# Kernel tuning notes

Hardware: AMD Instinct MI355X
Metric: run time of the kernel (lower is better)

The kernel has to match this reference:

```python
import jax, jax.numpy as jnp
import numpy as np

B, ENC, DEC, H, W = 8, 64, 128, 128, 128
NEG = -1e30  # masked-softmax fill


def _neighbors(x):
    """x: [B,H,W,C] -> [B,H,W,9,C] 3x3 neighborhood gather (zeros at borders)."""
    b, h, w, c = x.shape
    p = jnp.pad(x, ((0, 0), (1, 1), (1, 1), (0, 0)))
    return jnp.stack([p[:, r:r + h, c_:c_ + w, :] for r in range(3) for c_ in range(3)], axis=3)


def _neighbor_mask(h, w):
    """[H,W,9] bool: which of the 9 neighbors are in-bounds per pixel."""
    m = jnp.pad(jnp.ones((h, w), dtype=bool), ((1, 1), (1, 1)))
    return jnp.stack([m[r:r + h, c_:c_ + w] for r in range(3) for c_ in range(3)], axis=2)


def setup_inputs() -> dict:
    key = jax.random.key(0)
    ks = jax.random.split(key, 12)
    s = 0.05
    return {
        "encoder_features": jax.random.normal(ks[0], (B, ENC, H, W), jnp.float32),
        "decoder_features": jax.random.normal(ks[1], (B, DEC, H, W), jnp.float32),
        "W_enc": jax.random.normal(ks[2], (ENC, ENC), jnp.float32) * s,
        "b_enc": jax.random.normal(ks[3], (ENC,), jnp.float32) * s,
        "W_dec": jax.random.normal(ks[4], (DEC, ENC), jnp.float32) * s,
        "b_dec": jax.random.normal(ks[5], (ENC,), jnp.float32) * s,
        "W_agg": jax.random.normal(ks[6], (ENC, 1), jnp.float32) * s,
        "b_agg": jax.random.normal(ks[7], (1,), jnp.float32) * s,
        "W_attn": jax.random.normal(ks[8], (2 * ENC, ENC), jnp.float32) * s,
        "b_attn": jax.random.normal(ks[9], (ENC,), jnp.float32) * s,
        "conv_w": jax.random.normal(ks[10], (3, 3, DEC, ENC), jnp.float32) * s,  # HWIO
        "conv_b": jax.random.normal(ks[11], (ENC,), jnp.float32) * s,
    }


def reference(encoder_features, decoder_features, W_enc, b_enc, W_dec, b_dec,
              W_agg, b_agg, W_attn, b_attn, conv_w, conv_b):
    # NCHW -> NHWC (format_linear)
    enc = jnp.transpose(encoder_features, (0, 2, 3, 1))  # [B,H,W,ENC]
    dec = jnp.transpose(decoder_features, (0, 2, 3, 1))  # [B,H,W,DEC]

    q = dec @ W_dec + b_dec  # [B,H,W,ENC]
    k = enc @ W_enc + b_enc  # [B,H,W,ENC]
    vals = jax.lax.conv_general_dilated(
        dec, conv_w, window_strides=(1, 1), padding='SAME',
        dimension_numbers=('NHWC', 'HWIO', 'NHWC')) + conv_b  # [B,H,W,ENC]

    kn = _neighbors(k)    # [B,H,W,9,ENC]
    en = _neighbors(enc)  # [B,H,W,9,ENC]
    mask = _neighbor_mask(q.shape[1], q.shape[2])  # [H,W,9]

    # per-neighbor additive score: agg_encoder(tanh(query + key)) -> scalar
    scores = jnp.squeeze(jnp.tanh(q[:, :, :, None, :] + kn) @ W_agg, -1) + b_agg  # [B,H,W,9]
    scores = jnp.where(mask, scores, NEG)
    attn_w = jax.nn.softmax(scores, axis=-1)  # softmax over valid neighbors only
    attn_vec = jnp.einsum('bhwn,bhwnc->bhwc', attn_w, en)  # weighted sum of raw encoder feats

    cat = jnp.concatenate([vals, attn_vec], axis=-1)  # [B,H,W,2*ENC]
    out = cat @ W_attn + b_attn
    out = jnp.where(out >= 0, out, 0.2 * out)  # LeakyReLU(0.2)
    return jnp.transpose(out, (0, 3, 1, 2))  # back to NCHW
```

## Files before the change

kernel.cpp:

```cpp
#include <hip/hip_runtime.h>

#define BB 8
#define ENC_C 64
#define DEC_C 128
#define HH 128
#define WW 128

typedef unsigned short ushort_t;
typedef __attribute__((ext_vector_type(8))) short short8;
typedef __attribute__((ext_vector_type(4))) float f32x4;

static __device__ __forceinline__ ushort_t f2bf(float x) {
  unsigned int u = __builtin_bit_cast(unsigned int, x);
  u += 0x7fff + ((u >> 16) & 1);
  return (ushort_t)(u >> 16);
}
static __device__ __forceinline__ float bf2f(ushort_t v) {
  unsigned int u = ((unsigned int)v) << 16;
  return __builtin_bit_cast(float, u);
}

__global__ __launch_bounds__(64) void pack_w_kernel(
    const float* __restrict__ conv_w, const float* __restrict__ W_attn,
    const float* __restrict__ W_dec, const float* __restrict__ W_enc,
    ushort_t* __restrict__ packedC, ushort_t* __restrict__ packedA,
    ushort_t* __restrict__ packedQ, ushort_t* __restrict__ packedK)
{
  const int blk = blockIdx.x;
  const int l = threadIdx.x;
  const float* W;
  ushort_t* dst;
  int bb;
  if (blk < 144) {
    const int kstep = blk >> 2, nf = blk & 3;
    const int tap = kstep >> 2, dstep = kstep & 3;
    const int n = nf * 16 + (l & 15);
    const int dbase = dstep * 32 + (l >> 4) * 8;
    ushort_t v[8];
    #pragma unroll
    for (int j = 0; j < 8; ++j)
      v[j] = f2bf(conv_w[(tap * DEC_C + dbase + j) * 64 + n]);
    ushort_t* d = packedC + ((long)blk * 64 + l) * 8;
    #pragma unroll
    for (int j = 0; j < 8; ++j) d[j] = v[j];
    return;
  } else if (blk < 160) {
    W = W_attn; dst = packedA; bb = blk - 144;
  } else if (blk < 176) {
    W = W_dec;  dst = packedQ; bb = blk - 160;
  } else {
    W = W_enc;  dst = packedK; bb = blk - 176;
  }
  const int ks = bb >> 2, nf = bb & 3;
  const int n = nf * 16 + (l & 15);
  const int kbase = ks * 32 + (l >> 4) * 8;
  ushort_t v[8];
  #pragma unroll
  for (int j = 0; j < 8; ++j)
    v[j] = f2bf(W[(kbase + j) * 64 + n]);
  ushort_t* d = dst + ((long)bb * 64 + l) * 8;
  #pragma unroll
  for (int j = 0; j < 8; ++j) d[j] = v[j];
}

__global__ __launch_bounds__(256) void prep_kernel(
    const float* __restrict__ enc, const float* __restrict__ dec,
    const ushort_t* __restrict__ packedQ, const ushort_t* __restrict__ packedK,
    const float* __restrict__ b_enc, const float* __restrict__ b_dec,
    ushort_t* __restrict__ q_nhwc, ushort_t* __restrict__ k_nhwc,
    ushort_t* __restrict__ enc_t, ushort_t* __restrict__ dec_t)
{
  __shared__ float smem[WW * 68];
  const int bh = blockIdx.x;
  const int b = bh >> 7, h = bh & 127;
  const int tid = threadIdx.x;
  const int l = tid & 63;
  const int wv = tid >> 6;
  const int pix0 = wv * 32;
  const int col = l & 15, kg = l >> 4;

  #pragma unroll
  for (int i = 0; i < 32; ++i) {
    int idx = tid + i * 256;
    int cc = idx >> 7, wl = idx & 127;
    smem[wl * 68 + cc] = enc[((b * ENC_C + cc) * HH + h) * WW + wl];
  }
  __syncthreads();

  #pragma unroll
  for (int i = 0; i < 32; ++i) {
    int idx = tid + i * 256;
    int wl = idx >> 6, cc = idx & 63;
    enc_t[((long)bh * WW + wl) * 64 + cc] = f2bf(smem[wl * 68 + cc]);
  }

  f32x4 acck[2][4];
  #pragma unroll
  for (int mf = 0; mf < 2; ++mf)
    #pragma unroll
    for (int nf = 0; nf < 4; ++nf)
      acck[mf][nf] = (f32x4){0.f, 0.f, 0.f, 0.f};

  #pragma unroll
  for (int ks = 0; ks < 2; ++ks) {
    short8 afr[2];
    #pragma unroll
    for (int mf = 0; mf < 2; ++mf) {
      const int pix = pix0 + mf * 16 + col;
      const float4* p = (const float4*)&smem[pix * 68 + ks * 32 + kg * 8];
      float4 x0 = p[0], x1 = p[1];
      short8 v;
      v[0] = (short)f2bf(x0.x); v[1] = (short)f2bf(x0.y);
      v[2] = (short)f2bf(x0.z); v[3] = (short)f2bf(x0.w);
      v[4] = (short)f2bf(x1.x); v[5] = (short)f2bf(x1.y);
      v[6] = (short)f2bf(x1.z); v[7] = (short)f2bf(x1.w);
      afr[mf] = v;
    }
    #pragma unroll
    for (int nf = 0; nf < 4; ++nf) {
      const short8 bfr =
          *(const short8*)(packedK + ((long)(ks * 4 + nf) * 64 + l) * 8);
      acck[0][nf] = __builtin_amdgcn_mfma_f32_16x16x32_bf16(
          afr[0], bfr, acck[0][nf], 0, 0, 0);
      acck[1][nf] = __builtin_amdgcn_mfma_f32_16x16x32_bf16(
          afr[1], bfr, acck[1][nf], 0, 0, 0);
    }
  }
  #pragma unroll
  for (int mf = 0; mf < 2; ++mf)
    #pragma unroll
    for (int nf = 0; nf < 4; ++nf)
      #pragma unroll
      for (int r = 0; r < 4; ++r) {
        const int pix = pix0 + mf * 16 + kg * 4 + r;
        const int c = nf * 16 + col;
        k_nhwc[((long)bh * WW + pix) * 64 + c] = f2bf(acck[mf][nf][r] + b_enc[c]);
      }
  __syncthreads();

  f32x4 accq[2][4];
  #pragma unroll
  for (int mf = 0; mf < 2; ++mf)
    #pragma unroll
    for (int nf = 0; nf < 4; ++nf)
      accq[mf][nf] = (f32x4){0.f, 0.f, 0.f, 0.f};

  #pragma unroll
  for (int hf = 0; hf < 2; ++hf) {
    #pragma unroll
    for (int i = 0; i < 32; ++i) {
      int idx = tid + i * 256;
      int cc = idx >> 7, wl = idx & 127;
      smem[wl * 68 + cc] = dec[((b * DEC_C + hf * 64 + cc) * HH + h) * WW + wl];
    }
    __syncthreads();

    #pragma unroll
    for (int i = 0; i < 32; ++i) {
      int idx = tid + i * 256;
      int wl = idx >> 6, cc = idx & 63;
      dec_t[((long)bh * WW + wl) * DEC_C + hf * 64 + cc] =
          f2bf(smem[wl * 68 + cc]);
    }

    #pragma unroll
    for (int ks2 = 0; ks2 < 2; ++ks2) {
      const int ks = hf * 2 + ks2;
      short8 afr[2];
      #pragma unroll
      for (int mf = 0; mf < 2; ++mf) {
        const int pix = pix0 + mf * 16 + col;
        const float4* p = (const float4*)&smem[pix * 68 + ks2 * 32 + kg * 8];
        float4 x0 = p[0], x1 = p[1];
        short8 v;
        v[0] = (short)f2bf(x0.x); v[1] = (short)f2bf(x0.y);
        v[2] = (short)f2bf(x0.z); v[3] = (short)f2bf(x0.w);
        v[4] = (short)f2bf(x1.x); v[5] = (short)f2bf(x1.y);
        v[6] = (short)f2bf(x1.z); v[7] = (short)f2bf(x1.w);
        afr[mf] = v;
      }
      #pragma unroll
      for (int nf = 0; nf < 4; ++nf) {
        const short8 bfr =
            *(const short8*)(packedQ + ((long)(ks * 4 + nf) * 64 + l) * 8);
        accq[0][nf] = __builtin_amdgcn_mfma_f32_16x16x32_bf16(
            afr[0], bfr, accq[0][nf], 0, 0, 0);
        accq[1][nf] = __builtin_amdgcn_mfma_f32_16x16x32_bf16(
            afr[1], bfr, accq[1][nf], 0, 0, 0);
      }
    }
    __syncthreads();
  }

  #pragma unroll
  for (int mf = 0; mf < 2; ++mf)
    #pragma unroll
    for (int nf = 0; nf < 4; ++nf)
      #pragma unroll
      for (int r = 0; r < 4; ++r) {
        const int pix = pix0 + mf * 16 + kg * 4 + r;
        const int c = nf * 16 + col;
        q_nhwc[((long)bh * WW + pix) * 64 + c] = f2bf(accq[mf][nf][r] + b_dec[c]);
      }
}

__global__ __launch_bounds__(256) void attn_kernel(
    const ushort_t* __restrict__ q_nhwc, const ushort_t* __restrict__ k_nhwc,
    const ushort_t* __restrict__ enc_t, const float* __restrict__ W_agg,
    const float* __restrict__ b_agg, ushort_t* __restrict__ att)
{
  const int nwg = gridDim.x;
  const int cpx = nwg >> 3;
  const int bid = blockIdx.x;
  const int swz = (bid & 7) * cpx + (bid >> 3);
  const int t = swz * 256 + threadIdx.x;
  const int h = (t >> 7) & 127;
  const int w = t & 127;

  int off[9]; bool valid[9];
  #pragma unroll
  for (int n = 0; n < 9; ++n) {
    const int dh = n / 3 - 1, dw = n % 3 - 1;
    const int nh = h + dh, nw = w + dw;
    valid[n] = (nh >= 0 && nh < HH && nw >= 0 && nw < WW);
    const int nhc = min(max(nh, 0), HH - 1);
    const int nwc = min(max(nw, 0), WW - 1);
    off[n] = (t & ~16383) + nhc * WW + nwc;
  }

  const short8* qp = (const short8*)(q_nhwc + ((long)t << 6));
  const short8* kp[9];
  const short8* ep[9];
  #pragma unroll
  for (int n = 0; n < 9; ++n) {
    kp[n] = (const short8*)(k_nhwc + ((long)off[n] << 6));
    ep[n] = (const short8*)(enc_t + ((long)off[n] << 6));
  }

  float s[9];
  #pragma unroll
  for (int n = 0; n < 9; ++n) s[n] = 0.f;

  for (int ci = 0; ci < 4; ++ci) {
    const short8 qa = qp[2 * ci], qb = qp[2 * ci + 1];
    float wa[16];
    #pragma unroll
    for (int e = 0; e < 16; ++e) wa[e] = W_agg[ci * 16 + e];
    #pragma unroll
    for (int n = 0; n < 9; ++n) {
      const short8 ka = kp[n][2 * ci], kb = kp[n][2 * ci + 1];
      float sc = 0.f;
      #pragma unroll
      for (int e = 0; e < 8; ++e) {
        float x = bf2f((ushort_t)qa[e]) + bf2f((ushort_t)ka[e]);
        x = fminf(fmaxf(x, -15.f), 15.f);
        float z = __builtin_amdgcn_exp2f(x * 2.88539008f);
        float tt = __builtin_fmaf(-2.f, __builtin_amdgcn_rcpf(z + 1.f), 1.f);
        sc = __builtin_fmaf(tt, wa[e], sc);
      }
      #pragma unroll
      for (int e = 0; e < 8; ++e) {
        float x = bf2f((ushort_t)qb[e]) + bf2f((ushort_t)kb[e]);
        x = fminf(fmaxf(x, -15.f), 15.f);
        float z = __builtin_amdgcn_exp2f(x * 2.88539008f);
        float tt = __builtin_fmaf(-2.f, __builtin_amdgcn_rcpf(z + 1.f), 1.f);
        sc = __builtin_fmaf(tt, wa[8 + e], sc);
      }
      s[n] += sc;
    }
  }

  const float bagg = b_agg[0];
  float m = -1e30f;
  #pragma unroll
  for (int n = 0; n < 9; ++n) {
    s[n] = valid[n] ? (s[n] + bagg) : -1e30f;
    m = fmaxf(m, s[n]);
  }
  float attw[9]; float denom = 0.f;
  #pragma unroll
  for (int n = 0; n < 9; ++n) {
    attw[n] = __builtin_amdgcn_exp2f((s[n] - m) * 1.44269504f);
    denom += attw[n];
  }
  const float inv = __builtin_amdgcn_rcpf(denom);
  #pragma unroll
  for (int n = 0; n < 9; ++n) attw[n] *= inv;

  short8* op = (short8*)(att + ((long)t << 6));
  for (int ci = 0; ci < 4; ++ci) {
    float a16[16];
    #pragma unroll
    for (int e = 0; e < 16; ++e) a16[e] = 0.f;
    #pragma unroll
    for (int n = 0; n < 9; ++n) {
      const short8 ea = ep[n][2 * ci], eb = ep[n][2 * ci + 1];
      #pragma unroll
      for (int e = 0; e < 8; ++e)
        a16[e] = __builtin_fmaf(attw[n], bf2f((ushort_t)ea[e]), a16[e]);
      #pragma unroll
      for (int e = 0; e < 8; ++e)
        a16[8 + e] = __builtin_fmaf(attw[n], bf2f((ushort_t)eb[e]), a16[8 + e]);
    }
    short8 o0, o1;
    #pragma unroll
    for (int e = 0; e < 8; ++e) {
      o0[e] = (short)f2bf(a16[e]);
      o1[e] = (short)f2bf(a16[8 + e]);
    }
    op[2 * ci] = o0;
    op[2 * ci + 1] = o1;
  }
}

__global__ __launch_bounds__(256) void conv_out_kernel(
    const ushort_t* __restrict__ dec_t, const ushort_t* __restrict__ packedC,
    const float* __restrict__ conv_b, const ushort_t* __restrict__ attn_nhwc,
    const ushort_t* __restrict__ packedA, const float* __restrict__ b_attn,
    float* __restrict__ out)
{
  __shared__ ushort_t bsh[24576];
  ushort_t* vlds = bsh;
  const int nwg = gridDim.x;
  const int cpx = nwg >> 3;
  const int bid = blockIdx.x;
  const int grp = (bid & 7) * cpx + (bid >> 3);
  const int b = grp >> 6;
  const int h0 = (grp & 63) * 2;
  const int tid = threadIdx.x;
  const int l = tid & 63;
  const int wv = tid >> 6;
  const int pix0 = wv * 32;
  const int col = l & 15, kg = l >> 4;

  f32x4 acc[2][2][4];
  #pragma unroll
  for (int r = 0; r < 2; ++r)
    #pragma unroll
    for (int mf = 0; mf < 2; ++mf)
      #pragma unroll
      for (int nf = 0; nf < 4; ++nf)
        acc[r][mf][nf] = (f32x4){0.f, 0.f, 0.f, 0.f};

  #pragma unroll
  for (int kh = 0; kh < 3; ++kh) {
    __syncthreads();
    {
      const short8* src = (const short8*)(packedC + (long)kh * 24576);
      #pragma unroll
      for (int i = 0; i < 12; ++i)
        *(short8*)&bsh[(tid + i * 256) * 8] = src[tid + i * 256];
    }
    __syncthreads();

    const int hh0 = h0 + kh - 1;
    const bool v0 = (hh0 >= 0);
    const bool v1 = (h0 + kh <= HH - 1);
    const ushort_t* arow0 = dec_t + ((long)(b * HH + (v0 ? hh0 : 0)) * WW) * DEC_C;
    const ushort_t* arow1 = dec_t + ((long)(b * HH + (v1 ? hh0 + 1 : 0)) * WW) * DEC_C;

    #pragma unroll
    for (int ds = 0; ds < 4; ++ds) {
      const int d0 = ds * 32;
      short8 afr[2][3][2];
      #pragma unroll
      for (int kw = 0; kw < 3; ++kw)
        #pragma unroll
        for (int mf = 0; mf < 2; ++mf) {
          const int wp = pix0 + mf * 16 + col + kw - 1;
          const bool wok = (wp >= 0 && wp < WW);
          short8 z = {0, 0, 0, 0, 0, 0, 0, 0};
          afr[0][kw][mf] = (wok && v0)
              ? *(const short8*)(arow0 + (long)wp * DEC_C + d0 + kg * 8) : z;
          afr[1][kw][mf] = (wok && v1)
              ? *(const short8*)(arow1 + (long)wp * DEC_C + d0 + kg * 8) : z;
        }
      #pragma unroll
      for (int kw = 0; kw < 3; ++kw) {
        #pragma unroll
        for (int nf = 0; nf < 4; ++nf) {
          const short8 bfr =
              *(const short8*)&bsh[(((kw * 4 + ds) * 4 + nf) * 64 + l) * 8];
          #pragma unroll
          for (int r = 0; r < 2; ++r) {
            acc[r][0][nf] = __builtin_amdgcn_mfma_f32_16x16x32_bf16(
                afr[r][kw][0], bfr, acc[r][0][nf], 0, 0, 0);
            acc[r][1][nf] = __builtin_amdgcn_mfma_f32_16x16x32_bf16(
                afr[r][kw][1], bfr, acc[r][1][nf], 0, 0, 0);
          }
        }
      }
    }
  }

  __syncthreads();
  #pragma unroll
  for (int r = 0; r < 2; ++r)
    #pragma unroll
    for (int mf = 0; mf < 2; ++mf)
      #pragma unroll
      for (int nf = 0; nf < 4; ++nf)
        #pragma unroll
        for (int rr = 0; rr < 4; ++rr) {
          const int pix = pix0 + mf * 16 + kg * 4 + rr;
          const int c = nf * 16 + col;
          vlds[(r * WW + pix) * 72 + c] = f2bf(acc[r][mf][nf][rr] + conv_b[c]);
        }
  __syncthreads();

  for (int r = 0; r < 2; ++r) {
    const int bh = b * HH + h0 + r;
    f32x4 ao[4][2];
    #pragma unroll
    for (int mf = 0; mf < 4; ++mf)
      #pragma unroll
      for (int pf = 0; pf < 2; ++pf)
        ao[mf][pf] = (f32x4){0.f, 0.f, 0.f, 0.f};

    #pragma unroll
    for (int ks = 0; ks < 4; ++ks) {
      short8 bfr[2];
      #pragma unroll
      for (int pf = 0; pf < 2; ++pf) {
        const int pix = pix0 + pf * 16 + col;
        short8 v;
        if (ks < 2) {
          v = *(const short8*)&vlds[(r * WW + pix) * 72 + ks * 32 + kg * 8];
        } else {
          v = *(const short8*)(attn_nhwc + ((long)bh * WW + pix) * 64 +
                               (ks - 2) * 32 + kg * 8);
        }
        bfr[pf] = v;
      }
      #pragma unroll
      for (int mf = 0; mf < 4; ++mf) {
        const short8 afr =
            *(const short8*)(packedA + ((long)(ks * 4 + mf) * 64 + l) * 8);
        #pragma unroll
        for (int pf = 0; pf < 2; ++pf)
          ao[mf][pf] = __builtin_amdgcn_mfma_f32_16x16x32_bf16(
              afr, bfr[pf], ao[mf][pf], 0, 0, 0);
      }
    }

    #pragma unroll
    for (int mf = 0; mf < 4; ++mf)
      #pragma unroll
      for (int pf = 0; pf < 2; ++pf)
        #pragma unroll
        for (int rr = 0; rr < 4; ++rr) {
          const int n = mf * 16 + kg * 4 + rr;
          const int pix = pix0 + pf * 16 + col;
          float o = ao[mf][pf][rr] + b_attn[n];
          o = (o >= 0.f) ? o : 0.2f * o;
          out[((long)(b * ENC_C + n) * HH + (h0 + r)) * WW + pix] = o;
        }
  }
}

extern "C" void kernel_launch(void* const* d_in, const int* in_sizes, int n_in,
                              void* d_out, int out_size, void* d_ws, size_t ws_size,
                              hipStream_t stream) {
  const float* enc    = (const float*)d_in[0];
  const float* dec    = (const float*)d_in[1];
  const float* W_enc  = (const float*)d_in[2];
  const float* b_enc  = (const float*)d_in[3];
  const float* W_dec  = (const float*)d_in[4];
  const float* b_dec  = (const float*)d_in[5];
  const float* W_agg  = (const float*)d_in[6];
  const float* b_agg  = (const float*)d_in[7];
  const float* W_attn = (const float*)d_in[8];
  const float* b_attn = (const float*)d_in[9];
  const float* conv_w = (const float*)d_in[10];
  const float* conv_b = (const float*)d_in[11];
  float* out = (float*)d_out;

  const long npix = (long)BB * HH * WW;
  ushort_t* q_bf    = (ushort_t*)d_ws;
  ushort_t* k_bf    = q_bf + npix * 64;
  ushort_t* enc_t   = k_bf + npix * 64;
  ushort_t* dec_t   = enc_t + npix * 64;
  ushort_t* att     = dec_t + npix * 128;
  ushort_t* packedC = att + npix * 64;
  ushort_t* packedA = packedC + 144 * 64 * 8;
  ushort_t* packedQ = packedA + 16 * 64 * 8;
  ushort_t* packedK = packedQ + 16 * 64 * 8;

  hipLaunchKernelGGL(pack_w_kernel, dim3(184), dim3(64), 0, stream,
                     conv_w, W_attn, W_dec, W_enc, packedC, packedA, packedQ, packedK);
  hipLaunchKernelGGL(prep_kernel, dim3(BB * HH), dim3(256), 0, stream,
                     enc, dec, packedQ, packedK, b_enc, b_dec, q_bf, k_bf, enc_t, dec_t);
  hipLaunchKernelGGL(attn_kernel, dim3((int)(npix / 256)), dim3(256), 0, stream,
                     q_bf, k_bf, enc_t, W_agg, b_agg, att);
  hipLaunchKernelGGL(conv_out_kernel, dim3(BB * HH / 2), dim3(256), 0, stream,
                     dec_t, packedC, conv_b, att, packedA, b_attn, out);
}
```

Measured before the change: 145.7 us.

## Split attention per pixel across four lanes with shuffle-reduced scores

The attention kernel now assigns four threads per pixel, each handling a 16-channel slice, and combines the partial neighbor scores with xor shuffles before the softmax. This raises thread count fourfold, shortens each thread's serial work and register footprint, and makes adjacent lanes read contiguous channel chunks for better coalescing. In exchange, the softmax math is computed redundantly across the four lanes and shuffle traffic is added.

```diff
diff --git a/kernel.cpp b/kernel.cpp
--- a/kernel.cpp
+++ b/kernel.cpp
@@ -214,8 +214,10 @@
   const int bid = blockIdx.x;
   const int swz = (bid & 7) * cpx + (bid >> 3);
   const int t = swz * 256 + threadIdx.x;
-  const int h = (t >> 7) & 127;
-  const int w = t & 127;
+  const int pix = t >> 2;
+  const int cb = (t & 3) * 16;
+  const int h = (pix >> 7) & 127;
+  const int w = pix & 127;
 
   int off[9]; bool valid[9];
   #pragma unroll
@@ -225,49 +227,53 @@
     valid[n] = (nh >= 0 && nh < HH && nw >= 0 && nw < WW);
     const int nhc = min(max(nh, 0), HH - 1);
     const int nwc = min(max(nw, 0), WW - 1);
-    off[n] = (t & ~16383) + nhc * WW + nwc;
-  }
-
-  const short8* qp = (const short8*)(q_nhwc + ((long)t << 6));
-  const short8* kp[9];
-  const short8* ep[9];
+    off[n] = (pix & ~16383) + nhc * WW + nwc;
+  }
+
+  const short8* qp = (const short8*)(q_nhwc + ((long)pix << 6) + cb);
+  const short8 qa = qp[0], qb = qp[1];
+
+  float wa[16];
+  {
+    float4 w0 = *(const float4*)(W_agg + cb);
+    float4 w1 = *(const float4*)(W_agg + cb + 4);
+    float4 w2 = *(const float4*)(W_agg + cb + 8);
+    float4 w3 = *(const float4*)(W_agg + cb + 12);
+    wa[0]=w0.x; wa[1]=w0.y; wa[2]=w0.z; wa[3]=w0.w;
+    wa[4]=w1.x; wa[5]=w1.y; wa[6]=w1.z; wa[7]=w1.w;
+    wa[8]=w2.x; wa[9]=w2.y; wa[10]=w2.z; wa[11]=w2.w;
+    wa[12]=w3.x; wa[13]=w3.y; wa[14]=w3.z; wa[15]=w3.w;
+  }
+
+  float s[9];
   #pragma unroll
   for (int n = 0; n < 9; ++n) {
-    kp[n] = (const short8*)(k_nhwc + ((long)off[n] << 6));
-    ep[n] = (const short8*)(enc_t + ((long)off[n] << 6));
-  }
-
-  float s[9];
-  #pragma unroll
-  for (int n = 0; n < 9; ++n) s[n] = 0.f;
-
-  for (int ci = 0; ci < 4; ++ci) {
-    const short8 qa = qp[2 * ci], qb = qp[2 * ci + 1];
-    float wa[16];
-    #pragma unroll
-    for (int e = 0; e < 16; ++e) wa[e] = W_agg[ci * 16 + e];
-    #pragma unroll
-    for (int n = 0; n < 9; ++n) {
-      const short8 ka = kp[n][2 * ci], kb = kp[n][2 * ci + 1];
-      float sc = 0.f;
-      #pragma unroll
-      for (int e = 0; e < 8; ++e) {
-        float x = bf2f((ushort_t)qa[e]) + bf2f((ushort_t)ka[e]);
-        x = fminf(fmaxf(x, -15.f), 15.f);
-        float z = __builtin_amdgcn_exp2f(x * 2.88539008f);
-        float tt = __builtin_fmaf(-2.f, __builtin_amdgcn_rcpf(z + 1.f), 1.f);
-        sc = __builtin_fmaf(tt, wa[e], sc);
-      }
-      #pragma unroll
-      for (int e = 0; e < 8; ++e) {
-        float x = bf2f((ushort_t)qb[e]) + bf2f((ushort_t)kb[e]);
-        x = fminf(fmaxf(x, -15.f), 15.f);
-        float z = __builtin_amdgcn_exp2f(x * 2.88539008f);
-        float tt = __builtin_fmaf(-2.f, __builtin_amdgcn_rcpf(z + 1.f), 1.f);
-        sc = __builtin_fmaf(tt, wa[8 + e], sc);
-      }
-      s[n] += sc;
-    }
+    const short8* kp = (const short8*)(k_nhwc + ((long)off[n] << 6) + cb);
+    const short8 ka = kp[0], kb = kp[1];
+    float sc = 0.f;
+    #pragma unroll
+    for (int e = 0; e < 8; ++e) {
+      float x = bf2f((ushort_t)qa[e]) + bf2f((ushort_t)ka[e]);
+      x = fminf(fmaxf(x, -15.f), 15.f);
+      float z = __builtin_amdgcn_exp2f(x * 2.88539008f);
+      float tt = __builtin_fmaf(-2.f, __builtin_amdgcn_rcpf(z + 1.f), 1.f);
+      sc = __builtin_fmaf(tt, wa[e], sc);
+    }
+    #pragma unroll
+    for (int e = 0; e < 8; ++e) {
+      float x = bf2f((ushort_t)qb[e]) + bf2f((ushort_t)kb[e]);
+      x = fminf(fmaxf(x, -15.f), 15.f);
+      float z = __builtin_amdgcn_exp2f(x * 2.88539008f);
+      float tt = __builtin_fmaf(-2.f, __builtin_amdgcn_rcpf(z + 1.f), 1.f);
+      sc = __builtin_fmaf(tt, wa[8 + e], sc);
+    }
+    s[n] = sc;
+  }
+
+  #pragma unroll
+  for (int n = 0; n < 9; ++n) {
+    s[n] += __shfl_xor(s[n], 1);
+    s[n] += __shfl_xor(s[n], 2);
   }
 
   const float bagg = b_agg[0];
@@ -287,30 +293,29 @@
   #pragma unroll
   for (int n = 0; n < 9; ++n) attw[n] *= inv;
 
-  short8* op = (short8*)(att + ((long)t << 6));
-  for (int ci = 0; ci < 4; ++ci) {
-    float a16[16];
-    #pragma unroll
-    for (int e = 0; e < 16; ++e) a16[e] = 0.f;
-    #pragma unroll
-    for (int n = 0; n < 9; ++n) {
-      const short8 ea = ep[n][2 * ci], eb = ep[n][2 * ci + 1];
-      #pragma unroll
-      for (int e = 0; e < 8; ++e)
-        a16[e] = __builtin_fmaf(attw[n], bf2f((ushort_t)ea[e]), a16[e]);
-      #pragma unroll
-      for (int e = 0; e < 8; ++e)
-        a16[8 + e] = __builtin_fmaf(attw[n], bf2f((ushort_t)eb[e]), a16[8 + e]);
-    }
-    short8 o0, o1;
-    #pragma unroll
-    for (int e = 0; e < 8; ++e) {
-      o0[e] = (short)f2bf(a16[e]);
-      o1[e] = (short)f2bf(a16[8 + e]);
-    }
-    op[2 * ci] = o0;
-    op[2 * ci + 1] = o1;
-  }
+  float a16[16];
+  #pragma unroll
+  for (int e = 0; e < 16; ++e) a16[e] = 0.f;
+  #pragma unroll
+  for (int n = 0; n < 9; ++n) {
+    const short8* ep = (const short8*)(enc_t + ((long)off[n] << 6) + cb);
+    const short8 ea = ep[0], eb = ep[1];
+    #pragma unroll
+    for (int e = 0; e < 8; ++e)
+      a16[e] = __builtin_fmaf(attw[n], bf2f((ushort_t)ea[e]), a16[e]);
+    #pragma unroll
+    for (int e = 0; e < 8; ++e)
+      a16[8 + e] = __builtin_fmaf(attw[n], bf2f((ushort_t)eb[e]), a16[8 + e]);
+  }
+  short8 o0, o1;
+  #pragma unroll
+  for (int e = 0; e < 8; ++e) {
+    o0[e] = (short)f2bf(a16[e]);
+    o1[e] = (short)f2bf(a16[8 + e]);
+  }
+  short8* op = (short8*)(att + ((long)pix << 6) + cb);
+  op[0] = o0;
+  op[1] = o1;
 }
 
 __global__ __launch_bounds__(256) void conv_out_kernel(
@@ -490,7 +495,7 @@
                      conv_w, W_attn, W_dec, W_enc, packedC, packedA, packedQ, packedK);
   hipLaunchKernelGGL(prep_kernel, dim3(BB * HH), dim3(256), 0, stream,
                      enc, dec, packedQ, packedK, b_enc, b_dec, q_bf, k_bf, enc_t, dec_t);
-  hipLaunchKernelGGL(attn_kernel, dim3((int)(npix / 256)), dim3(256), 0, stream,
+  hipLaunchKernelGGL(attn_kernel, dim3((int)(npix * 4 / 256)), dim3(256), 0, stream,
                      q_bf, k_bf, enc_t, W_agg, b_agg, att);
   hipLaunchKernelGGL(conv_out_kernel, dim3(BB * HH / 2), dim3(256), 0, stream,
                      dec_t, packedC, conv_b, att, packedA, b_attn, out);
```

Result: faster. 123.0 us (-15.6%).
